# Optimization experiments

Measured on AMD Instinct MI355X. Metric: run time of the kernel, lower is better.

Reference implementation:

```python
import jax, jax.numpy as jnp
import numpy as np

DEPTH = 2
EPS = 1e-12

def _l2norm(x, axis=-1):
    n = jnp.sqrt(jnp.sum(x * x, axis=axis, keepdims=True))
    return x / jnp.maximum(n, EPS)

def setup_inputs() -> dict:
    key = jax.random.key(0)
    k1, k2, k3, k4, k5 = jax.random.split(key, 5)
    N, D, R, E = 50000, 100, 1000, 800000
    features = jax.random.normal(k1, (N, D), dtype=jnp.float32)
    rel_emb = jax.random.normal(k2, (R, D), dtype=jnp.float32)
    none_relation = jax.random.normal(k3, (D,), dtype=jnp.float32)
    # edge list sorted by destination row (matches coalesced sparse layout
    # assumed by the original: softmax values align with edge order)
    rows = jnp.sort(jax.random.randint(k4, (E,), 0, N))
    cols = jax.random.randint(k5, (E,), 0, N)
    adj_index = jnp.stack([rows, cols], axis=1).astype(jnp.int64)
    return {"features": features, "rel_emb": rel_emb,
            "adj_index": adj_index, "none_relation": none_relation}

def reference(features, rel_emb, adj_index, none_relation):
    N = features.shape[0]
    rows = adj_index[:, 0]  # destination (softmax segment, scatter target)
    cols = adj_index[:, 1]  # neighbor (gather source)
    feats = jnp.tanh(features)
    outputs = [feats]
    nr = _l2norm(none_relation, axis=0)  # [D]
    for _ in range(DEPTH):
        neighs = feats[cols]                      # [E, D] gather
        score = -jnp.einsum('ed,d->e', _l2norm(neighs), nr)  # [E]
        # sparse softmax over each destination row's edges
        m = jax.ops.segment_max(score, rows, num_segments=N)
        e = jnp.exp(score - m[rows])
        denom = jax.ops.segment_sum(e, rows, num_segments=N)
        att = e / denom[rows]                     # [E]
        new_feats = jax.ops.segment_sum(neighs * att[:, None], rows,
                                        num_segments=N)  # [N, D]
        feats = jnp.tanh(new_feats)
        outputs.append(feats)
    return jnp.concatenate(outputs, axis=1)  # [N, D*(DEPTH+1)]
```

## Files before the change

### kernel.cpp

```cpp
#include <hip/hip_runtime.h>
#include <hip/hip_fp16.h>
#include <math.h>

#define D_FEAT 100
#define ROW_STRIDE 300
#define ROWB 208u

__device__ __forceinline__ float fast_tanh(float x) {
    float ax = fabsf(x);
    float e  = __expf(2.f * ax);
    float t  = 1.f - 2.f / (e + 1.f);
    return copysignf(t, x);
}

__device__ __forceinline__ unsigned pack_f16x2(float a, float b) {
    __half2 h = __floats2half2_rn(a, b);
    union { __half2 h; unsigned u; } cvt; cvt.h = h;
    return cvt.u;
}

__device__ __forceinline__ float half_reduce(float v) {
    #pragma unroll
    for (int off = 16; off; off >>= 1) v += __shfl_xor(v, off, 64);
    return v;
}

__global__ __launch_bounds__(256) void tanh_score_kernel(
    const float* __restrict__ features,
    float* __restrict__ out,
    unsigned long long* __restrict__ tab0,
    float* __restrict__ escore0,
    const float* __restrict__ none_rel,
    const int* __restrict__ adj,
    int* __restrict__ startArr,
    int E, int N)
{
    int gtid = blockIdx.x * blockDim.x + threadIdx.x;
    if (gtid <= N) {
        if (gtid == N) startArr[N] = E;
        else {
            int lo = 0, hi = E;
            while (lo < hi) {
                int mid = (lo + hi) >> 1;
                if (adj[2 * mid] < gtid) lo = mid + 1; else hi = mid;
            }
            startArr[gtid] = lo;
        }
    }

    int waveId = gtid >> 6;
    int lane = threadIdx.x & 63;
    int h32  = lane >> 5;
    int l    = lane & 31;
    int n    = waveId * 2 + h32;
    const bool valid_n = (n < N);
    const bool fact = valid_n && (l >= 1) && (l <= 25);

    float x0 = 0.f, x1 = 0.f, x2 = 0.f, x3 = 0.f;
    if (fact) {
        float4 f = ((const float4*)(features + (size_t)n * D_FEAT))[l - 1];
        x0 = fast_tanh(f.x); x1 = fast_tanh(f.y);
        x2 = fast_tanh(f.z); x3 = fast_tanh(f.w);
        ((float4*)(out + (size_t)n * ROW_STRIDE))[l - 1] = make_float4(x0, x1, x2, x3);
    }
    if (tab0 && valid_n) {
        char* row = (char*)tab0 + (size_t)n * ROWB;
        if (l >= 1 && l <= 25) {
            unsigned long long q = (unsigned long long)pack_f16x2(x0, x1) |
                                   ((unsigned long long)pack_f16x2(x2, x3) << 32);
            *(unsigned long long*)(row + 8 * (l - 1)) = q;
        } else if (l == 26) {
            *(unsigned long long*)(row + 200) = 0ULL;
        }
    }

    float nx = 0.f, ny = 0.f, nz = 0.f, nw = 0.f;
    if (l >= 1 && l <= 25) {
        float4 v = ((const float4*)none_rel)[l - 1];
        nx = v.x; ny = v.y; nz = v.z; nw = v.w;
    }
    float ss = half_reduce(nx * nx + ny * ny + nz * nz + nw * nw);
    float inv_nr = 1.f / fmaxf(sqrtf(ss), 1e-12f);

    float dot = half_reduce(x0 * nx + x1 * ny + x2 * nz + x3 * nw) * inv_nr;
    float sq  = half_reduce(x0 * x0 + x1 * x1 + x2 * x2 + x3 * x3);
    if (l == 0 && valid_n) {
        float es = __expf(-dot / fmaxf(sqrtf(sq), 1e-12f));
        escore0[n] = es;
    }
}

template <bool WRITE_TAB>
__global__ __launch_bounds__(256) void attn16_kernel(
    const unsigned long long* __restrict__ tab,
    float* __restrict__ outp,
    unsigned long long* __restrict__ tab_out,
    const int2* __restrict__ adj2,
    const int* __restrict__ start,
    const float* __restrict__ esc_in,
    float* __restrict__ esc_out,
    const float* __restrict__ none_rel,
    int N)
{
    const int waveId = (int)((blockIdx.x * blockDim.x + threadIdx.x) >> 6);
    const int lane = threadIdx.x & 63;
    const int h32  = lane >> 5;
    const int l    = lane & 31;
    const int base = h32 << 5;
    const int n    = waveId * 2 + h32;
    const bool valid_n = (n < N);

    const bool act  = (l < 26);
    const int  wh   = (act && l >= 13) ? 1 : 0;
    const int  sub  = act ? (l - 13 * wh) : 0;
    const bool actA = (l < 13);

    int e0 = 0, e1 = 0;
    if (valid_n) { e0 = start[n]; e1 = start[n + 1]; }
    const int deg = e1 - e0;
    int maxdeg = deg;
    { int o = __shfl_xor(maxdeg, 32, 64); maxdeg = maxdeg > o ? maxdeg : o; }

    int   c0 = 0, c1 = 0;
    float w0 = 0.f, w1 = 0.f;
    if (l < deg)      { c0 = adj2[e0 + l].y;      w0 = esc_in[c0]; }
    if (l + 32 < deg) { c1 = adj2[e0 + l + 32].y; w1 = esc_in[c1]; }

    float dsum = half_reduce(w0 + w1);

    const char* tb = (const char*)tab;
    const unsigned suboff = (unsigned)(sub * 16);

    float a0=0.f,a1=0.f,a2=0.f,a3=0.f,a4=0.f,a5=0.f,a6=0.f,a7=0.f;

#define ATTN16_PASS(CSTAGE, WSTAGE, SRC)                                      \
    {                                                                         \
        int   c = __shfl((CSTAGE), base + (SRC) + wh, 64);                    \
        float w = __shfl((WSTAGE), base + (SRC) + wh, 64);                    \
        const uint4 v = *(const uint4*)(tb + (size_t)((unsigned)c * ROWB + suboff)); \
        const __half2* hv = (const __half2*)&v;                               \
        a0 = fmaf(__low2float(hv[0]),  w, a0);                                \
        a1 = fmaf(__high2float(hv[0]), w, a1);                                \
        a2 = fmaf(__low2float(hv[1]),  w, a2);                                \
        a3 = fmaf(__high2float(hv[1]), w, a3);                                \
        a4 = fmaf(__low2float(hv[2]),  w, a4);                                \
        a5 = fmaf(__high2float(hv[2]), w, a5);                                \
        a6 = fmaf(__low2float(hv[3]),  w, a6);                                \
        a7 = fmaf(__high2float(hv[3]), w, a7);                                \
    }

    const int cap1 = maxdeg < 32 ? maxdeg : 32;
    for (int r = 0; r < cap1; r += 8) {
        #pragma unroll
        for (int j = 0; j < 4; ++j) {
            ATTN16_PASS(c0, w0, r + 2 * j)
        }
    }
    const int cap2 = maxdeg < 64 ? maxdeg : 64;
    for (int r = 32; r < cap2; r += 8) {
        #pragma unroll
        for (int j = 0; j < 4; ++j) {
            ATTN16_PASS(c1, w1, r + 2 * j - 32)
        }
    }
#undef ATTN16_PASS

    for (int e = e0 + 64; e < e1; ++e) {
        int   c = adj2[e].y;
        float w = esc_in[c];
        const uint4 v = *(const uint4*)(tb + (size_t)((unsigned)c * ROWB + suboff));
        const __half2* hv = (const __half2*)&v;
        if (actA) {
            a0 = fmaf(__low2float(hv[0]),  w, a0);
            a1 = fmaf(__high2float(hv[0]), w, a1);
            a2 = fmaf(__low2float(hv[1]),  w, a2);
            a3 = fmaf(__high2float(hv[1]), w, a3);
            a4 = fmaf(__low2float(hv[2]),  w, a4);
            a5 = fmaf(__high2float(hv[2]), w, a5);
            a6 = fmaf(__low2float(hv[3]),  w, a6);
            a7 = fmaf(__high2float(hv[3]), w, a7);
        }
        dsum += w;
    }

    const int partner = base + (actA ? l + 13 : (act ? l - 13 : l));
    a0 += __shfl(a0, partner, 64);
    a1 += __shfl(a1, partner, 64);
    a2 += __shfl(a2, partner, 64);
    a3 += __shfl(a3, partner, 64);
    a4 += __shfl(a4, partner, 64);
    a5 += __shfl(a5, partner, 64);
    a6 += __shfl(a6, partner, 64);
    a7 += __shfl(a7, partner, 64);

    const float inv_d = (deg > 0) ? 1.f / dsum : 0.f;
    float r0 = fast_tanh(a0 * inv_d);
    float r1 = fast_tanh(a1 * inv_d);
    float r2 = fast_tanh(a2 * inv_d);
    float r3 = fast_tanh(a3 * inv_d);
    float r4 = fast_tanh(a4 * inv_d);
    float r5 = fast_tanh(a5 * inv_d);
    float r6 = fast_tanh(a6 * inv_d);
    float r7 = fast_tanh(a7 * inv_d);
    if (!actA) { r0=r1=r2=r3=r4=r5=r6=r7=0.f; }

    if (valid_n && actA) {
        float4* orow = (float4*)(outp + (size_t)n * ROW_STRIDE);
        orow[2*l] = make_float4(r0, r1, r2, r3);
        if (l < 12)
            orow[2*l + 1] = make_float4(r4, r5, r6, r7);
        if constexpr (WRITE_TAB) {
            uint4* trow = (uint4*)((char*)tab_out + (size_t)n * ROWB);
            trow[l] = make_uint4(pack_f16x2(r0, r1), pack_f16x2(r2, r3),
                                 pack_f16x2(r4, r5), pack_f16x2(r6, r7));
        }
    }

    if constexpr (WRITE_TAB) {
        float n0=0.f,n1=0.f,n2=0.f,n3=0.f,n4=0.f,n5=0.f,n6=0.f,n7=0.f;
        if (actA) {
            float4 u = *(const float4*)(none_rel + 8 * l);
            n0=u.x; n1=u.y; n2=u.z; n3=u.w;
            if (l < 12) {
                float4 v2 = *(const float4*)(none_rel + 8 * l + 4);
                n4=v2.x; n5=v2.y; n6=v2.z; n7=v2.w;
            }
        }
        float ss = half_reduce(n0*n0+n1*n1+n2*n2+n3*n3+n4*n4+n5*n5+n6*n6+n7*n7);
        float inv_nr = 1.f / fmaxf(sqrtf(ss), 1e-12f);
        float dot = half_reduce(r0*n0+r1*n1+r2*n2+r3*n3+r4*n4+r5*n5+r6*n6+r7*n7) * inv_nr;
        float sq  = half_reduce(r0*r0+r1*r1+r2*r2+r3*r3+r4*r4+r5*r5+r6*r6+r7*r7);
        if (l == 0 && valid_n) {
            float es = __expf(-dot / fmaxf(sqrtf(sq), 1e-12f));
            esc_out[n] = es;
        }
    }
}

__global__ __launch_bounds__(256) void attn_f32_kernel(
    const float* __restrict__ prev,
    float* __restrict__ outp,
    const int2* __restrict__ adj2,
    const int* __restrict__ start,
    const float* __restrict__ escore_in,
    float* __restrict__ escore_out,
    const float* __restrict__ none_rel,
    int N)
{
    int waveId = (int)((blockIdx.x * blockDim.x + threadIdx.x) >> 6);
    int lane = threadIdx.x & 63;
    int h32  = lane >> 5;
    int l    = lane & 31;
    int n    = waveId * 2 + h32;
    const bool valid_n = (n < N);
    const bool fact = valid_n && (l >= 1) && (l <= 25);
    const int base = h32 << 5;

    int e0 = 0, e1 = 0;
    if (valid_n) { e0 = start[n]; e1 = start[n + 1]; }
    const int deg = e1 - e0;

    int   c0 = 0, c1 = 0;
    float w0 = 0.f, w1 = 0.f;
    if (l < deg)      { c0 = adj2[e0 + l].y;      w0 = escore_in[c0]; }
    if (l + 32 < deg) { c1 = adj2[e0 + l + 32].y; w1 = escore_in[c1]; }

    int maxdeg = deg;
    { int o = __shfl_xor(maxdeg, 32, 64); maxdeg = maxdeg > o ? maxdeg : o; }

    float d_acc = 0.f, a0 = 0.f, a1 = 0.f, a2 = 0.f, a3 = 0.f;
    const int cap1 = maxdeg < 32 ? maxdeg : 32;
    for (int r = 0; r < cap1; r += 8) {
        #pragma unroll
        for (int j = 0; j < 8; ++j) {
            int   i = r + j;
            int   c = __shfl(c0, base + i, 64);
            float w = __shfl(w0, base + i, 64);
            float p0 = 0.f, p1 = 0.f, p2 = 0.f, p3 = 0.f;
            if (fact && (i < deg)) {
                float4 v = ((const float4*)(prev + (size_t)c * ROW_STRIDE))[l - 1];
                p0 = v.x; p1 = v.y; p2 = v.z; p3 = v.w;
            }
            if (i >= deg) w = 0.f;
            d_acc += w;
            a0 += w * p0; a1 += w * p1; a2 += w * p2; a3 += w * p3;
        }
    }
    const int cap2 = maxdeg < 64 ? maxdeg : 64;
    for (int r = 32; r < cap2; r += 8) {
        #pragma unroll
        for (int j = 0; j < 8; ++j) {
            int   i = r + j;
            int   c = __shfl(c1, base + i - 32, 64);
            float w = __shfl(w1, base + i - 32, 64);
            float p0 = 0.f, p1 = 0.f, p2 = 0.f, p3 = 0.f;
            if (fact && (i < deg)) {
                float4 v = ((const float4*)(prev + (size_t)c * ROW_STRIDE))[l - 1];
                p0 = v.x; p1 = v.y; p2 = v.z; p3 = v.w;
            }
            if (i >= deg) w = 0.f;
            d_acc += w;
            a0 += w * p0; a1 += w * p1; a2 += w * p2; a3 += w * p3;
        }
    }
    for (int e = e0 + 64; e < e1; ++e) {
        int c = adj2[e].y;
        float w = escore_in[c];
        float p0 = 0.f, p1 = 0.f, p2 = 0.f, p3 = 0.f;
        if (fact) {
            float4 v = ((const float4*)(prev + (size_t)c * ROW_STRIDE))[l - 1];
            p0 = v.x; p1 = v.y; p2 = v.z; p3 = v.w;
        }
        d_acc += w;
        a0 += w * p0; a1 += w * p1; a2 += w * p2; a3 += w * p3;
    }

    const float inv_d = (deg > 0) ? 1.f / d_acc : 0.f;
    float r0 = fast_tanh(a0 * inv_d);
    float r1 = fast_tanh(a1 * inv_d);
    float r2 = fast_tanh(a2 * inv_d);
    float r3 = fast_tanh(a3 * inv_d);
    if (fact) {
        ((float4*)(outp + (size_t)n * ROW_STRIDE))[l - 1] = make_float4(r0, r1, r2, r3);
    } else {
        r0 = r1 = r2 = r3 = 0.f;
    }

    if (escore_out) {
        float nx = 0.f, ny = 0.f, nz = 0.f, nw = 0.f;
        if (l >= 1 && l <= 25) {
            float4 v = ((const float4*)none_rel)[l - 1];
            nx = v.x; ny = v.y; nz = v.z; nw = v.w;
        }
        float ss = half_reduce(nx * nx + ny * ny + nz * nz + nw * nw);
        float inv_nr = 1.f / fmaxf(sqrtf(ss), 1e-12f);
        float dot = half_reduce(r0 * nx + r1 * ny + r2 * nz + r3 * nw) * inv_nr;
        float sq  = half_reduce(r0 * r0 + r1 * r1 + r2 * r2 + r3 * r3);
        if (l == 0 && valid_n) {
            float es = __expf(-dot / fmaxf(sqrtf(sq), 1e-12f));
            escore_out[n] = es;
        }
    }
}

extern "C" void kernel_launch(void* const* d_in, const int* in_sizes, int n_in,
                              void* d_out, int out_size, void* d_ws, size_t ws_size,
                              hipStream_t stream) {
    const float* features = (const float*)d_in[0];
    const int*   adj      = (const int*)d_in[2];
    const float* none_rel = (const float*)d_in[3];
    float* out = (float*)d_out;

    const int N = in_sizes[0] / D_FEAT;
    const int E = in_sizes[2] / 2;

    size_t off = 0;
    auto take = [&](size_t bytes) { size_t o = off; off = (off + bytes + 15) & ~(size_t)15; return o; };
    char* w = (char*)d_ws;
    int*   start   = (int*)  (w + take(sizeof(int)   * (size_t)(N + 1)));
    float* escore0 = (float*)(w + take(sizeof(float) * (size_t)N));
    float* escore1 = (float*)(w + take(sizeof(float) * (size_t)N));
    size_t tab_off0 = take((size_t)N * ROWB);
    size_t tab_off1 = take((size_t)N * ROWB);
    const bool use_tab = (ws_size >= off);
    unsigned long long* tab0 = use_tab ? (unsigned long long*)(w + tab_off0) : nullptr;
    unsigned long long* tab1 = use_tab ? (unsigned long long*)(w + tab_off1) : nullptr;

    const int pairs = (N + 1) / 2;
    const int node_blocks = (pairs * 64 + 255) / 256;
    const int2* adj2 = (const int2*)adj;

    tanh_score_kernel<<<node_blocks, 256, 0, stream>>>(features, out, tab0,
                                                       escore0, none_rel,
                                                       adj, start, E, N);
    if (use_tab) {
        attn16_kernel<true><<<node_blocks, 256, 0, stream>>>(
            tab0, out + D_FEAT, tab1, adj2, start, escore0, escore1, none_rel, N);
        attn16_kernel<false><<<node_blocks, 256, 0, stream>>>(
            tab1, out + 2 * D_FEAT, nullptr, adj2, start, escore1, nullptr, none_rel, N);
    } else {
        attn_f32_kernel<<<node_blocks, 256, 0, stream>>>(
            out, out + D_FEAT, adj2, start, escore0, escore1, none_rel, N);
        attn_f32_kernel<<<node_blocks, 256, 0, stream>>>(
            out + D_FEAT, out + 2 * D_FEAT, adj2, start, escore1, nullptr, none_rel, N);
    }
}
```

Measured before the change: 159.4 us.

## Map one node per wave with four concurrent edge groups in fp16 attention

Replaces the two-nodes-per-wave attention kernel with one node per wave. Lanes are split into four groups of 13, and each group gathers a different neighbor's fp16 row, so four row loads are in flight per pass and 16 edges are handled per loop iteration. Partial sums are combined with two cross-lane shuffle steps. This targets latency-bound gathers and the divergence caused by pairing nodes of different degree, at the cost of launching twice as many waves. The 12 leftover lanes also issue unused loads.

After: 168.2 us. 1.06x slower.

```diff
diff --git a/kernel.cpp b/kernel.cpp
--- a/kernel.cpp
+++ b/kernel.cpp
@@ -22,6 +22,11 @@
 __device__ __forceinline__ float half_reduce(float v) {
     #pragma unroll
     for (int off = 16; off; off >>= 1) v += __shfl_xor(v, off, 64);
+    return v;
+}
+__device__ __forceinline__ float full_reduce(float v) {
+    #pragma unroll
+    for (int off = 32; off; off >>= 1) v += __shfl_xor(v, off, 64);
     return v;
 }
 
@@ -91,7 +96,7 @@
 }
 
 template <bool WRITE_TAB>
-__global__ __launch_bounds__(256) void attn16_kernel(
+__global__ __launch_bounds__(256) void attn4_kernel(
     const unsigned long long* __restrict__ tab,
     float* __restrict__ outp,
     unsigned long long* __restrict__ tab_out,
@@ -102,75 +107,89 @@
     const float* __restrict__ none_rel,
     int N)
 {
-    const int waveId = (int)((blockIdx.x * blockDim.x + threadIdx.x) >> 6);
+    const int n    = (int)((blockIdx.x * blockDim.x + threadIdx.x) >> 6);
     const int lane = threadIdx.x & 63;
-    const int h32  = lane >> 5;
-    const int l    = lane & 31;
-    const int base = h32 << 5;
-    const int n    = waveId * 2 + h32;
+    const int g    = lane / 13;
+    const int li   = lane - 13 * g;
+    const bool actA = (lane < 13);
     const bool valid_n = (n < N);
-
-    const bool act  = (l < 26);
-    const int  wh   = (act && l >= 13) ? 1 : 0;
-    const int  sub  = act ? (l - 13 * wh) : 0;
-    const bool actA = (l < 13);
 
     int e0 = 0, e1 = 0;
     if (valid_n) { e0 = start[n]; e1 = start[n + 1]; }
     const int deg = e1 - e0;
-    int maxdeg = deg;
-    { int o = __shfl_xor(maxdeg, 32, 64); maxdeg = maxdeg > o ? maxdeg : o; }
-
-    int   c0 = 0, c1 = 0;
-    float w0 = 0.f, w1 = 0.f;
-    if (l < deg)      { c0 = adj2[e0 + l].y;      w0 = esc_in[c0]; }
-    if (l + 32 < deg) { c1 = adj2[e0 + l + 32].y; w1 = esc_in[c1]; }
-
-    float dsum = half_reduce(w0 + w1);
+
+    int cst = 0; float wst = 0.f;
+    if (lane < deg) { cst = adj2[e0 + lane].y; wst = esc_in[cst]; }
+
+    float dsum = full_reduce(wst);
 
     const char* tb = (const char*)tab;
-    const unsigned suboff = (unsigned)(sub * 16);
+    const unsigned suboff = (unsigned)(li * 16);
 
     float a0=0.f,a1=0.f,a2=0.f,a3=0.f,a4=0.f,a5=0.f,a6=0.f,a7=0.f;
 
-#define ATTN16_PASS(CSTAGE, WSTAGE, SRC)                                      \
-    {                                                                         \
-        int   c = __shfl((CSTAGE), base + (SRC) + wh, 64);                    \
-        float w = __shfl((WSTAGE), base + (SRC) + wh, 64);                    \
-        const uint4 v = *(const uint4*)(tb + (size_t)((unsigned)c * ROWB + suboff)); \
-        const __half2* hv = (const __half2*)&v;                               \
-        a0 = fmaf(__low2float(hv[0]),  w, a0);                                \
-        a1 = fmaf(__high2float(hv[0]), w, a1);                                \
-        a2 = fmaf(__low2float(hv[1]),  w, a2);                                \
-        a3 = fmaf(__high2float(hv[1]), w, a3);                                \
-        a4 = fmaf(__low2float(hv[2]),  w, a4);                                \
-        a5 = fmaf(__high2float(hv[2]), w, a5);                                \
-        a6 = fmaf(__low2float(hv[3]),  w, a6);                                \
-        a7 = fmaf(__high2float(hv[3]), w, a7);                                \
-    }
-
-    const int cap1 = maxdeg < 32 ? maxdeg : 32;
-    for (int r = 0; r < cap1; r += 8) {
-        #pragma unroll
-        for (int j = 0; j < 4; ++j) {
-            ATTN16_PASS(c0, w0, r + 2 * j)
-        }
-    }
-    const int cap2 = maxdeg < 64 ? maxdeg : 64;
-    for (int r = 32; r < cap2; r += 8) {
-        #pragma unroll
-        for (int j = 0; j < 4; ++j) {
-            ATTN16_PASS(c1, w1, r + 2 * j - 32)
-        }
-    }
-#undef ATTN16_PASS
+    const int cap = deg < 64 ? deg : 64;
+    const int npass = (cap + 3) >> 2;
+
+    for (int p0 = 0; p0 < npass; p0 += 4) {
+        const int i0 = (4 * (p0 + 0) + g) & 63;
+        const int i1 = (4 * (p0 + 1) + g) & 63;
+        const int i2 = (4 * (p0 + 2) + g) & 63;
+        const int i3 = (4 * (p0 + 3) + g) & 63;
+        int   cc0 = __shfl(cst, i0, 64), cc1 = __shfl(cst, i1, 64);
+        int   cc2 = __shfl(cst, i2, 64), cc3 = __shfl(cst, i3, 64);
+        float ww0 = __shfl(wst, i0, 64), ww1 = __shfl(wst, i1, 64);
+        float ww2 = __shfl(wst, i2, 64), ww3 = __shfl(wst, i3, 64);
+
+        const uint4 v0 = *(const uint4*)(tb + (size_t)((unsigned)cc0 * ROWB + suboff));
+        const uint4 v1 = *(const uint4*)(tb + (size_t)((unsigned)cc1 * ROWB + suboff));
+        const uint4 v2 = *(const uint4*)(tb + (size_t)((unsigned)cc2 * ROWB + suboff));
+        const uint4 v3 = *(const uint4*)(tb + (size_t)((unsigned)cc3 * ROWB + suboff));
+
+        const __half2* h0 = (const __half2*)&v0;
+        const __half2* h1 = (const __half2*)&v1;
+        const __half2* h2 = (const __half2*)&v2;
+        const __half2* h3 = (const __half2*)&v3;
+        a0 = fmaf(__low2float(h0[0]),  ww0, a0);
+        a1 = fmaf(__high2float(h0[0]), ww0, a1);
+        a2 = fmaf(__low2float(h0[1]),  ww0, a2);
+        a3 = fmaf(__high2float(h0[1]), ww0, a3);
+        a4 = fmaf(__low2float(h0[2]),  ww0, a4);
+        a5 = fmaf(__high2float(h0[2]), ww0, a5);
+        a6 = fmaf(__low2float(h0[3]),  ww0, a6);
+        a7 = fmaf(__high2float(h0[3]), ww0, a7);
+        a0 = fmaf(__low2float(h1[0]),  ww1, a0);
+        a1 = fmaf(__high2float(h1[0]), ww1, a1);
+        a2 = fmaf(__low2float(h1[1]),  ww1, a2);
+        a3 = fmaf(__high2float(h1[1]), ww1, a3);
+        a4 = fmaf(__low2float(h1[2]),  ww1, a4);
+        a5 = fmaf(__high2float(h1[2]), ww1, a5);
+        a6 = fmaf(__low2float(h1[3]),  ww1, a6);
+        a7 = fmaf(__high2float(h1[3]), ww1, a7);
+        a0 = fmaf(__low2float(h2[0]),  ww2, a0);
+        a1 = fmaf(__high2float(h2[0]), ww2, a1);
+        a2 = fmaf(__low2float(h2[1]),  ww2, a2);
+        a3 = fmaf(__high2float(h2[1]), ww2, a3);
+        a4 = fmaf(__low2float(h2[2]),  ww2, a4);
+        a5 = fmaf(__high2float(h2[2]), ww2, a5);
+        a6 = fmaf(__low2float(h2[3]),  ww2, a6);
+        a7 = fmaf(__high2float(h2[3]), ww2, a7);
+        a0 = fmaf(__low2float(h3[0]),  ww3, a0);
+        a1 = fmaf(__high2float(h3[0]), ww3, a1);
+        a2 = fmaf(__low2float(h3[1]),  ww3, a2);
+        a3 = fmaf(__high2float(h3[1]), ww3, a3);
+        a4 = fmaf(__low2float(h3[2]),  ww3, a4);
+        a5 = fmaf(__high2float(h3[2]), ww3, a5);
+        a6 = fmaf(__low2float(h3[3]),  ww3, a6);
+        a7 = fmaf(__high2float(h3[3]), ww3, a7);
+    }
 
     for (int e = e0 + 64; e < e1; ++e) {
         int   c = adj2[e].y;
         float w = esc_in[c];
         const uint4 v = *(const uint4*)(tb + (size_t)((unsigned)c * ROWB + suboff));
         const __half2* hv = (const __half2*)&v;
-        if (actA) {
+        if (g == 0) {
             a0 = fmaf(__low2float(hv[0]),  w, a0);
             a1 = fmaf(__high2float(hv[0]), w, a1);
             a2 = fmaf(__low2float(hv[1]),  w, a2);
@@ -183,15 +202,16 @@
         dsum += w;
     }
 
-    const int partner = base + (actA ? l + 13 : (act ? l - 13 : l));
-    a0 += __shfl(a0, partner, 64);
-    a1 += __shfl(a1, partner, 64);
-    a2 += __shfl(a2, partner, 64);
-    a3 += __shfl(a3, partner, 64);
-    a4 += __shfl(a4, partner, 64);
-    a5 += __shfl(a5, partner, 64);
-    a6 += __shfl(a6, partner, 64);
-    a7 += __shfl(a7, partner, 64);
+    const int pr1 = (lane + 26) & 63;
+    a0 += __shfl(a0, pr1, 64); a1 += __shfl(a1, pr1, 64);
+    a2 += __shfl(a2, pr1, 64); a3 += __shfl(a3, pr1, 64);
+    a4 += __shfl(a4, pr1, 64); a5 += __shfl(a5, pr1, 64);
+    a6 += __shfl(a6, pr1, 64); a7 += __shfl(a7, pr1, 64);
+    const int pr2 = (lane + 13) & 63;
+    a0 += __shfl(a0, pr2, 64); a1 += __shfl(a1, pr2, 64);
+    a2 += __shfl(a2, pr2, 64); a3 += __shfl(a3, pr2, 64);
+    a4 += __shfl(a4, pr2, 64); a5 += __shfl(a5, pr2, 64);
+    a6 += __shfl(a6, pr2, 64); a7 += __shfl(a7, pr2, 64);
 
     const float inv_d = (deg > 0) ? 1.f / dsum : 0.f;
     float r0 = fast_tanh(a0 * inv_d);
@@ -205,6 +225,7 @@
     if (!actA) { r0=r1=r2=r3=r4=r5=r6=r7=0.f; }
 
     if (valid_n && actA) {
+        const int l = lane;
         float4* orow = (float4*)(outp + (size_t)n * ROW_STRIDE);
         orow[2*l] = make_float4(r0, r1, r2, r3);
         if (l < 12)
@@ -217,6 +238,7 @@
     }
 
     if constexpr (WRITE_TAB) {
+        const int l = lane;
         float n0=0.f,n1=0.f,n2=0.f,n3=0.f,n4=0.f,n5=0.f,n6=0.f,n7=0.f;
         if (actA) {
             float4 u = *(const float4*)(none_rel + 8 * l);
@@ -230,7 +252,7 @@
         float inv_nr = 1.f / fmaxf(sqrtf(ss), 1e-12f);
         float dot = half_reduce(r0*n0+r1*n1+r2*n2+r3*n3+r4*n4+r5*n5+r6*n6+r7*n7) * inv_nr;
         float sq  = half_reduce(r0*r0+r1*r1+r2*r2+r3*r3+r4*r4+r5*r5+r6*r6+r7*r7);
-        if (l == 0 && valid_n) {
+        if (lane == 0 && valid_n) {
             float es = __expf(-dot / fmaxf(sqrtf(sq), 1e-12f));
             esc_out[n] = es;
         }
@@ -374,9 +396,10 @@
                                                        escore0, none_rel,
                                                        adj, start, E, N);
     if (use_tab) {
-        attn16_kernel<true><<<node_blocks, 256, 0, stream>>>(
+        const int attn_blocks = (N * 64 + 255) / 256;
+        attn4_kernel<true><<<attn_blocks, 256, 0, stream>>>(
             tab0, out + D_FEAT, tab1, adj2, start, escore0, escore1, none_rel, N);
-        attn16_kernel<false><<<node_blocks, 256, 0, stream>>>(
+        attn4_kernel<false><<<attn_blocks, 256, 0, stream>>>(
             tab1, out + 2 * D_FEAT, nullptr, adj2, start, escore1, nullptr, none_rel, N);
     } else {
         attn_f32_kernel<<<node_blocks, 256, 0, stream>>>(
```

## Quantize gather table to 8-bit and compact column indices

Applied to the files above, without the earlier changes.

Replaces the fp16 feature table (208-byte rows) with an 8-bit offset-quantized table (112-byte rows), so the random neighbor gathers move about half as many bytes. The attention kernel is rebuilt around 7-lane groups that each read 16-byte chunks and handle 4 edges per pass, with a two-step shuffle reduction and the dequantization offset folded into the normalization. Column indices are also copied into a compact int array in the first kernel, so the attention kernels stop reading the interleaved 64-bit adjacency pairs. The cost is lower feature precision (about 1/127 step) and an extra E-sized workspace write.

New measurement: 161.5 us. No clear change (+1.3%).

```diff
diff --git a/kernel.cpp b/kernel.cpp
--- a/kernel.cpp
+++ b/kernel.cpp
@@ -4,7 +4,7 @@
 
 #define D_FEAT 100
 #define ROW_STRIDE 300
-#define ROWB 208u
+#define ROWB 112u
 
 __device__ __forceinline__ float fast_tanh(float x) {
     float ax = fabsf(x);
@@ -13,10 +13,12 @@
     return copysignf(t, x);
 }
 
-__device__ __forceinline__ unsigned pack_f16x2(float a, float b) {
-    __half2 h = __floats2half2_rn(a, b);
-    union { __half2 h; unsigned u; } cvt; cvt.h = h;
-    return cvt.u;
+__device__ __forceinline__ unsigned pb4(float x0, float x1, float x2, float x3) {
+    unsigned b0 = (unsigned)(int)rintf(fmaf(x0, 127.f, 128.f));
+    unsigned b1 = (unsigned)(int)rintf(fmaf(x1, 127.f, 128.f));
+    unsigned b2 = (unsigned)(int)rintf(fmaf(x2, 127.f, 128.f));
+    unsigned b3 = (unsigned)(int)rintf(fmaf(x3, 127.f, 128.f));
+    return b0 | (b1 << 8) | (b2 << 16) | (b3 << 24);
 }
 
 __device__ __forceinline__ float half_reduce(float v) {
@@ -28,14 +30,16 @@
 __global__ __launch_bounds__(256) void tanh_score_kernel(
     const float* __restrict__ features,
     float* __restrict__ out,
-    unsigned long long* __restrict__ tab0,
+    unsigned char* __restrict__ tab0,
     float* __restrict__ escore0,
     const float* __restrict__ none_rel,
     const int* __restrict__ adj,
     int* __restrict__ startArr,
+    int* __restrict__ cols,
     int E, int N)
 {
     int gtid = blockIdx.x * blockDim.x + threadIdx.x;
+    if (gtid < E && cols) cols[gtid] = adj[2 * gtid + 1];
     if (gtid <= N) {
         if (gtid == N) startArr[N] = E;
         else {
@@ -64,13 +68,12 @@
         ((float4*)(out + (size_t)n * ROW_STRIDE))[l - 1] = make_float4(x0, x1, x2, x3);
     }
     if (tab0 && valid_n) {
-        char* row = (char*)tab0 + (size_t)n * ROWB;
+        unsigned char* row = tab0 + (size_t)n * ROWB;
         if (l >= 1 && l <= 25) {
-            unsigned long long q = (unsigned long long)pack_f16x2(x0, x1) |
-                                   ((unsigned long long)pack_f16x2(x2, x3) << 32);
-            *(unsigned long long*)(row + 8 * (l - 1)) = q;
+            *(unsigned*)(row + 4 * (l - 1)) = pb4(x0, x1, x2, x3);
         } else if (l == 26) {
-            *(unsigned long long*)(row + 200) = 0ULL;
+            *(unsigned*)(row + 100) = 0x80808080u;
+            *(unsigned long long*)(row + 104) = 0x8080808080808080ull;
         }
     }
 
@@ -91,11 +94,11 @@
 }
 
 template <bool WRITE_TAB>
-__global__ __launch_bounds__(256) void attn16_kernel(
-    const unsigned long long* __restrict__ tab,
+__global__ __launch_bounds__(256) void attn8_kernel(
+    const unsigned char* __restrict__ tab,
     float* __restrict__ outp,
-    unsigned long long* __restrict__ tab_out,
-    const int2* __restrict__ adj2,
+    unsigned char* __restrict__ tab_out,
+    const int* __restrict__ cols,
     const int* __restrict__ start,
     const float* __restrict__ esc_in,
     float* __restrict__ esc_out,
@@ -105,15 +108,14 @@
     const int waveId = (int)((blockIdx.x * blockDim.x + threadIdx.x) >> 6);
     const int lane = threadIdx.x & 63;
     const int h32  = lane >> 5;
-    const int l    = lane & 31;
+    const int hl   = lane & 31;
     const int base = h32 << 5;
     const int n    = waveId * 2 + h32;
     const bool valid_n = (n < N);
 
-    const bool act  = (l < 26);
-    const int  wh   = (act && l >= 13) ? 1 : 0;
-    const int  sub  = act ? (l - 13 * wh) : 0;
-    const bool actA = (l < 13);
+    const int grp = hl / 7;
+    const int li  = hl - 7 * grp;
+    const unsigned suboff = (unsigned)(li * 16);
 
     int e0 = 0, e1 = 0;
     if (valid_n) { e0 = start[n]; e1 = start[n + 1]; }
@@ -123,114 +125,124 @@
 
     int   c0 = 0, c1 = 0;
     float w0 = 0.f, w1 = 0.f;
-    if (l < deg)      { c0 = adj2[e0 + l].y;      w0 = esc_in[c0]; }
-    if (l + 32 < deg) { c1 = adj2[e0 + l + 32].y; w1 = esc_in[c1]; }
+    if (hl < deg)      { c0 = cols[e0 + hl];      w0 = esc_in[c0]; }
+    if (hl + 32 < deg) { c1 = cols[e0 + hl + 32]; w1 = esc_in[c1]; }
 
     float dsum = half_reduce(w0 + w1);
 
-    const char* tb = (const char*)tab;
-    const unsigned suboff = (unsigned)(sub * 16);
-
-    float a0=0.f,a1=0.f,a2=0.f,a3=0.f,a4=0.f,a5=0.f,a6=0.f,a7=0.f;
-
-#define ATTN16_PASS(CSTAGE, WSTAGE, SRC)                                      \
+    float a[16];
+    #pragma unroll
+    for (int k = 0; k < 16; ++k) a[k] = 0.f;
+
+#define ACC16(V, W)                                                           \
     {                                                                         \
-        int   c = __shfl((CSTAGE), base + (SRC) + wh, 64);                    \
-        float w = __shfl((WSTAGE), base + (SRC) + wh, 64);                    \
-        const uint4 v = *(const uint4*)(tb + (size_t)((unsigned)c * ROWB + suboff)); \
-        const __half2* hv = (const __half2*)&v;                               \
-        a0 = fmaf(__low2float(hv[0]),  w, a0);                                \
-        a1 = fmaf(__high2float(hv[0]), w, a1);                                \
-        a2 = fmaf(__low2float(hv[1]),  w, a2);                                \
-        a3 = fmaf(__high2float(hv[1]), w, a3);                                \
-        a4 = fmaf(__low2float(hv[2]),  w, a4);                                \
-        a5 = fmaf(__high2float(hv[2]), w, a5);                                \
-        a6 = fmaf(__low2float(hv[3]),  w, a6);                                \
-        a7 = fmaf(__high2float(hv[3]), w, a7);                                \
+        unsigned _d;                                                          \
+        _d = (V).x;                                                           \
+        a[0]  = fmaf((float)(_d & 255u),         (W), a[0]);                  \
+        a[1]  = fmaf((float)((_d >> 8) & 255u),  (W), a[1]);                  \
+        a[2]  = fmaf((float)((_d >> 16) & 255u), (W), a[2]);                  \
+        a[3]  = fmaf((float)(_d >> 24),          (W), a[3]);                  \
+        _d = (V).y;                                                           \
+        a[4]  = fmaf((float)(_d & 255u),         (W), a[4]);                  \
+        a[5]  = fmaf((float)((_d >> 8) & 255u),  (W), a[5]);                  \
+        a[6]  = fmaf((float)((_d >> 16) & 255u), (W), a[6]);                  \
+        a[7]  = fmaf((float)(_d >> 24),          (W), a[7]);                  \
+        _d = (V).z;                                                           \
+        a[8]  = fmaf((float)(_d & 255u),         (W), a[8]);                  \
+        a[9]  = fmaf((float)((_d >> 8) & 255u),  (W), a[9]);                  \
+        a[10] = fmaf((float)((_d >> 16) & 255u), (W), a[10]);                 \
+        a[11] = fmaf((float)(_d >> 24),          (W), a[11]);                 \
+        _d = (V).w;                                                           \
+        a[12] = fmaf((float)(_d & 255u),         (W), a[12]);                 \
+        a[13] = fmaf((float)((_d >> 8) & 255u),  (W), a[13]);                 \
+        a[14] = fmaf((float)((_d >> 16) & 255u), (W), a[14]);                 \
+        a[15] = fmaf((float)(_d >> 24),          (W), a[15]);                 \
+    }
+
+#define BATCH8(CST, WST, SRCB)                                                \
+    {                                                                         \
+        const int sA = base + (SRCB) + grp;                                   \
+        const int sB = base + (SRCB) + 4 + grp;                               \
+        int   cA = __shfl((CST), sA, 64), cB = __shfl((CST), sB, 64);         \
+        float wA = __shfl((WST), sA, 64), wB = __shfl((WST), sB, 64);         \
+        const uint4 vA = *(const uint4*)(tab + (size_t)((unsigned)cA * ROWB + suboff)); \
+        const uint4 vB = *(const uint4*)(tab + (size_t)((unsigned)cB * ROWB + suboff)); \
+        ACC16(vA, wA) ACC16(vB, wB)                                           \
     }
 
     const int cap1 = maxdeg < 32 ? maxdeg : 32;
-    for (int r = 0; r < cap1; r += 8) {
+    for (int r = 0; r < cap1; r += 8) BATCH8(c0, w0, r)
+    const int cap2 = maxdeg < 64 ? maxdeg : 64;
+    for (int r = 32; r < cap2; r += 8) BATCH8(c1, w1, r - 32)
+#undef BATCH8
+
+    for (int e = e0 + 64; e < e1; ++e) {
+        int   c = cols[e];
+        float w = esc_in[c];
+        const uint4 v = *(const uint4*)(tab + (size_t)((unsigned)c * ROWB + suboff));
+        if (grp == 0) ACC16(v, w)
+        dsum += w;
+    }
+#undef ACC16
+
+    const int p1 = base + hl + ((hl < 14) ? 14 : 0);
+    #pragma unroll
+    for (int k = 0; k < 16; ++k) a[k] += __shfl(a[k], p1, 64);
+    const int p2 = base + hl + ((hl < 7) ? 7 : 0);
+    #pragma unroll
+    for (int k = 0; k < 16; ++k) a[k] += __shfl(a[k], p2, 64);
+
+    const float invd = (deg > 0) ? 1.f / (127.f * dsum) : 0.f;
+    const float bsh  = (deg > 0) ? (-128.f / 127.f) : 0.f;
+    float r[16];
+    #pragma unroll
+    for (int k = 0; k < 16; ++k) {
+        r[k] = fast_tanh(fmaf(a[k], invd, bsh));
+        if (!(valid_n) || (16 * hl + k) >= 100) r[k] = 0.f;
+    }
+
+    if (valid_n && hl < 7) {
+        float4* orow = (float4*)(outp + (size_t)n * ROW_STRIDE);
         #pragma unroll
         for (int j = 0; j < 4; ++j) {
-            ATTN16_PASS(c0, w0, r + 2 * j)
-        }
-    }
-    const int cap2 = maxdeg < 64 ? maxdeg : 64;
-    for (int r = 32; r < cap2; r += 8) {
+            if (j == 0 || hl < 6)
+                orow[4 * hl + j] = make_float4(r[4*j], r[4*j+1], r[4*j+2], r[4*j+3]);
+        }
+        if constexpr (WRITE_TAB) {
+            unsigned char* trow = tab_out + (size_t)n * ROWB;
+            *(uint4*)(trow + 16 * hl) = make_uint4(
+                pb4(r[0],  r[1],  r[2],  r[3]),
+                pb4(r[4],  r[5],  r[6],  r[7]),
+                pb4(r[8],  r[9],  r[10], r[11]),
+                pb4(r[12], r[13], r[14], r[15]));
+        }
+    }
+
+    if constexpr (WRITE_TAB) {
+        float nn[16];
         #pragma unroll
-        for (int j = 0; j < 4; ++j) {
-            ATTN16_PASS(c1, w1, r + 2 * j - 32)
-        }
-    }
-#undef ATTN16_PASS
-
-    for (int e = e0 + 64; e < e1; ++e) {
-        int   c = adj2[e].y;
-        float w = esc_in[c];
-        const uint4 v = *(const uint4*)(tb + (size_t)((unsigned)c * ROWB + suboff));
-        const __half2* hv = (const __half2*)&v;
-        if (actA) {
-            a0 = fmaf(__low2float(hv[0]),  w, a0);
-            a1 = fmaf(__high2float(hv[0]), w, a1);
-            a2 = fmaf(__low2float(hv[1]),  w, a2);
-            a3 = fmaf(__high2float(hv[1]), w, a3);
-            a4 = fmaf(__low2float(hv[2]),  w, a4);
-            a5 = fmaf(__high2float(hv[2]), w, a5);
-            a6 = fmaf(__low2float(hv[3]),  w, a6);
-            a7 = fmaf(__high2float(hv[3]), w, a7);
-        }
-        dsum += w;
-    }
-
-    const int partner = base + (actA ? l + 13 : (act ? l - 13 : l));
-    a0 += __shfl(a0, partner, 64);
-    a1 += __shfl(a1, partner, 64);
-    a2 += __shfl(a2, partner, 64);
-    a3 += __shfl(a3, partner, 64);
-    a4 += __shfl(a4, partner, 64);
-    a5 += __shfl(a5, partner, 64);
-    a6 += __shfl(a6, partner, 64);
-    a7 += __shfl(a7, partner, 64);
-
-    const float inv_d = (deg > 0) ? 1.f / dsum : 0.f;
-    float r0 = fast_tanh(a0 * inv_d);
-    float r1 = fast_tanh(a1 * inv_d);
-    float r2 = fast_tanh(a2 * inv_d);
-    float r3 = fast_tanh(a3 * inv_d);
-    float r4 = fast_tanh(a4 * inv_d);
-    float r5 = fast_tanh(a5 * inv_d);
-    float r6 = fast_tanh(a6 * inv_d);
-    float r7 = fast_tanh(a7 * inv_d);
-    if (!actA) { r0=r1=r2=r3=r4=r5=r6=r7=0.f; }
-
-    if (valid_n && actA) {
-        float4* orow = (float4*)(outp + (size_t)n * ROW_STRIDE);
-        orow[2*l] = make_float4(r0, r1, r2, r3);
-        if (l < 12)
-            orow[2*l + 1] = make_float4(r4, r5, r6, r7);
-        if constexpr (WRITE_TAB) {
-            uint4* trow = (uint4*)((char*)tab_out + (size_t)n * ROWB);
-            trow[l] = make_uint4(pack_f16x2(r0, r1), pack_f16x2(r2, r3),
-                                 pack_f16x2(r4, r5), pack_f16x2(r6, r7));
-        }
-    }
-
-    if constexpr (WRITE_TAB) {
-        float n0=0.f,n1=0.f,n2=0.f,n3=0.f,n4=0.f,n5=0.f,n6=0.f,n7=0.f;
-        if (actA) {
-            float4 u = *(const float4*)(none_rel + 8 * l);
-            n0=u.x; n1=u.y; n2=u.z; n3=u.w;
-            if (l < 12) {
-                float4 v2 = *(const float4*)(none_rel + 8 * l + 4);
-                n4=v2.x; n5=v2.y; n6=v2.z; n7=v2.w;
+        for (int k = 0; k < 16; ++k) nn[k] = 0.f;
+        if (hl < 7) {
+            #pragma unroll
+            for (int j = 0; j < 4; ++j) {
+                if (j == 0 || hl < 6) {
+                    float4 u = *(const float4*)(none_rel + 16 * hl + 4 * j);
+                    nn[4*j] = u.x; nn[4*j+1] = u.y; nn[4*j+2] = u.z; nn[4*j+3] = u.w;
+                }
             }
         }
-        float ss = half_reduce(n0*n0+n1*n1+n2*n2+n3*n3+n4*n4+n5*n5+n6*n6+n7*n7);
+        float ssl = 0.f, dotl = 0.f, sql = 0.f;
+        #pragma unroll
+        for (int k = 0; k < 16; ++k) {
+            ssl  += nn[k] * nn[k];
+            dotl += r[k] * nn[k];
+            sql  += r[k] * r[k];
+        }
+        float ss  = half_reduce(ssl);
         float inv_nr = 1.f / fmaxf(sqrtf(ss), 1e-12f);
-        float dot = half_reduce(r0*n0+r1*n1+r2*n2+r3*n3+r4*n4+r5*n5+r6*n6+r7*n7) * inv_nr;
-        float sq  = half_reduce(r0*r0+r1*r1+r2*r2+r3*r3+r4*r4+r5*r5+r6*r6+r7*r7);
-        if (l == 0 && valid_n) {
+        float dot = half_reduce(dotl) * inv_nr;
+        float sq  = half_reduce(sql);
+        if (hl == 0 && valid_n) {
             float es = __expf(-dot / fmaxf(sqrtf(sq), 1e-12f));
             esc_out[n] = es;
         }
@@ -360,11 +372,12 @@
     int*   start   = (int*)  (w + take(sizeof(int)   * (size_t)(N + 1)));
     float* escore0 = (float*)(w + take(sizeof(float) * (size_t)N));
     float* escore1 = (float*)(w + take(sizeof(float) * (size_t)N));
+    int*   cols    = (int*)  (w + take(sizeof(int)   * (size_t)E));
     size_t tab_off0 = take((size_t)N * ROWB);
     size_t tab_off1 = take((size_t)N * ROWB);
     const bool use_tab = (ws_size >= off);
-    unsigned long long* tab0 = use_tab ? (unsigned long long*)(w + tab_off0) : nullptr;
-    unsigned long long* tab1 = use_tab ? (unsigned long long*)(w + tab_off1) : nullptr;
+    unsigned char* tab0 = use_tab ? (unsigned char*)(w + tab_off0) : nullptr;
+    unsigned char* tab1 = use_tab ? (unsigned char*)(w + tab_off1) : nullptr;
 
     const int pairs = (N + 1) / 2;
     const int node_blocks = (pairs * 64 + 255) / 256;
@@ -372,12 +385,14 @@
 
     tanh_score_kernel<<<node_blocks, 256, 0, stream>>>(features, out, tab0,
                                                        escore0, none_rel,
-                                                       adj, start, E, N);
+                                                       adj, start,
+                                                       use_tab ? cols : nullptr,
+                                                       E, N);
     if (use_tab) {
-        attn16_kernel<true><<<node_blocks, 256, 0, stream>>>(
-            tab0, out + D_FEAT, tab1, adj2, start, escore0, escore1, none_rel, N);
-        attn16_kernel<false><<<node_blocks, 256, 0, stream>>>(
-            tab1, out + 2 * D_FEAT, nullptr, adj2, start, escore1, nullptr, none_rel, N);
+        attn8_kernel<true><<<node_blocks, 256, 0, stream>>>(
+            tab0, out + D_FEAT, tab1, cols, start, escore0, escore1, none_rel, N);
+        attn8_kernel<false><<<node_blocks, 256, 0, stream>>>(
+            tab1, out + 2 * D_FEAT, nullptr, cols, start, escore1, nullptr, none_rel, N);
     } else {
         attn_f32_kernel<<<node_blocks, 256, 0, stream>>>(
             out, out + D_FEAT, adj2, start, escore0, escore1, none_rel, N);
```
